# Kernel tuning notes

Hardware: AMD Instinct MI355X
Metric: run time of the kernel (lower is better)

Reference implementation:

```python
import jax, jax.numpy as jnp
import numpy as np


def setup_inputs() -> dict:
    key = jax.random.key(0)
    ks = jax.random.split(key, 7)
    B, C, W, H = 4, 256, 64, 64
    C8 = C // 8
    return {
        "x": jax.random.normal(ks[0], (B, C, W, H), dtype=jnp.float32),
        "Wq": jax.random.normal(ks[1], (C8, C), dtype=jnp.float32) * 0.05,
        "bq": jax.random.normal(ks[2], (C8,), dtype=jnp.float32) * 0.05,
        "Wk": jax.random.normal(ks[3], (C8, C), dtype=jnp.float32) * 0.05,
        "bk": jax.random.normal(ks[4], (C8,), dtype=jnp.float32) * 0.05,
        "Wv": jax.random.normal(ks[5], (C, C), dtype=jnp.float32) * 0.05,
        "bv": jax.random.normal(ks[6], (C,), dtype=jnp.float32) * 0.05,
    }


def reference(x, Wq, bq, Wk, bk, Wv, bv):
    B, C, W, H = x.shape
    N = W * H
    xf = x.reshape(B, C, N)  # flatten spatial dims
    # 1x1 convs == per-position linear projections
    q = jnp.einsum('oc,bcn->bno', Wq, xf) + bq            # (B, N, C/8)
    k = jnp.einsum('oc,bcn->bon', Wk, xf) + bk[None, :, None]  # (B, C/8, N)
    # attention scores (B, N, N); original applies softmax over dim=1
    attn = jax.nn.softmax(jnp.einsum('bno,bom->bnm', q, k), axis=1)
    v = jnp.einsum('oc,bcn->bno', Wv, xf) + bv            # (B, N, C)
    out = jnp.einsum('bnm,bmc->bnc', attn, v)             # (B, N, C)
    # faithful to original: raw view of (B, N, C) as (B, C, W, H)
    return out.reshape(B, C, W, H)
```

## Files before the change

kernel.cpp:

```cpp
#include <hip/hip_runtime.h>
#include <math.h>

#define NB 4
#define CC 256
#define CO 32
#define NN 4096
#define MU 320
#define LOG2E 1.44269504088896f

typedef __attribute__((ext_vector_type(4))) float f4;
typedef __attribute__((ext_vector_type(8))) short s8;
typedef __attribute__((ext_vector_type(8))) unsigned short us8;
typedef __attribute__((ext_vector_type(2))) unsigned int u2;
typedef __attribute__((ext_vector_type(4))) unsigned int u4i;

__device__ __forceinline__ unsigned short f2bf(float f) {
    unsigned int u = __float_as_uint(f);
    u = (u + 0x7FFFu + ((u >> 16) & 1u)) >> 16;
    return (unsigned short)u;
}
__device__ __forceinline__ unsigned int cvtpk(float lo, float hi) {
    unsigned int r;
    asm("v_cvt_pk_bf16_f32 %0, %1, %2" : "=v"(r) : "v"(lo), "v"(hi));
    return r;
}
__device__ __forceinline__ int swz128(int row, int colByte) {
    return row * 128 + (colByte ^ ((row & 7) << 4));
}

union s8u4 { s8 s; u4i u; };

__global__ __launch_bounds__(256) void prepw_kernel(
    const float* __restrict__ Wq, const float* __restrict__ bq,
    const float* __restrict__ Wk, const float* __restrict__ bk,
    const float* __restrict__ Wv, const float* __restrict__ bv,
    unsigned short* __restrict__ Wb, float* __restrict__ fb)
{
    const int t = threadIdx.x;
    #pragma unroll
    for (int i = 0; i < 4; ++i) {
        const int e = blockIdx.x * 1024 + i * 256 + t;
        const int u = e >> 8, c = e & 255;
        float val = (u < 32) ? Wq[u * 256 + c]
                  : (u < 64) ? Wk[(u - 32) * 256 + c]
                             : Wv[(u - 64) * 256 + c];
        Wb[e] = f2bf(val);
    }
    if (blockIdx.x == 0) {
        for (int u = t; u < MU; u += 256)
            fb[u] = (u < 32) ? bq[u] : (u < 64) ? bk[u - 32] : bv[u - 64];
    }
}

__global__ __launch_bounds__(256) void projf_kernel(
    const float* __restrict__ x, const unsigned short* __restrict__ Wb,
    const float* __restrict__ fb,
    unsigned short* __restrict__ qb, unsigned short* __restrict__ kb,
    unsigned short* __restrict__ vtb)
{
    __shared__ float xl[32][260];

    const int t   = threadIdx.x;
    const int b   = blockIdx.x >> 7;
    const int nbl = blockIdx.x & 127;
    const int n0  = nbl * 32;

    {
        const int nl = t & 7;
        const int c8 = t >> 3;
        #pragma unroll
        for (int pass = 0; pass < 8; ++pass) {
            const int c = c8 + pass * 32;
            f4 xv = *reinterpret_cast<const f4*>(x + ((size_t)(b * CC + c)) * NN + n0 + nl * 4);
            #pragma unroll
            for (int j = 0; j < 4; ++j) xl[nl * 4 + j][c] = xv[j];
        }
    }
    __syncthreads();

    const int w    = t >> 6;
    const int l    = t & 63;
    const int l15  = l & 15;
    const int g4   = l >> 4;
    const int nw   = w & 1;
    const int uw   = w >> 1;
    const int nloc = nw * 16 + l15;
    const int n    = n0 + nloc;

    s8 bfr[8];
    #pragma unroll
    for (int kk = 0; kk < 8; ++kk) {
        f4 a  = *reinterpret_cast<const f4*>(&xl[nloc][kk * 32 + g4 * 8]);
        f4 c2 = *reinterpret_cast<const f4*>(&xl[nloc][kk * 32 + g4 * 8 + 4]);
        s8u4 tmp;
        tmp.u = (u4i){ cvtpk(a[0], a[1]), cvtpk(a[2], a[3]),
                       cvtpk(c2[0], c2[1]), cvtpk(c2[2], c2[3]) };
        bfr[kk] = tmp.s;
    }

    const f4 z = {0.f, 0.f, 0.f, 0.f};
    unsigned short* qrow = qb + ((size_t)(b * NN + n)) * CO;
    unsigned short* krow = kb + ((size_t)(b * NN + n)) * CO;

    #pragma unroll
    for (int i = 0; i < 10; ++i) {
        const int u0 = (uw * 10 + i) * 16;
        f4 acc = z;
        #pragma unroll
        for (int kk = 0; kk < 8; ++kk) {
            s8 af = *reinterpret_cast<const s8*>(Wb + (size_t)(u0 + l15) * CC + kk * 32 + g4 * 8);
            acc = __builtin_amdgcn_mfma_f32_16x16x32_bf16(af, bfr[kk], acc, 0, 0, 0);
        }
        f4 bias4 = *reinterpret_cast<const f4*>(fb + u0 + g4 * 4);
        if (u0 < 32) {
            u2 pw = { cvtpk((acc[0] + bias4[0]) * LOG2E, (acc[1] + bias4[1]) * LOG2E),
                      cvtpk((acc[2] + bias4[2]) * LOG2E, (acc[3] + bias4[3]) * LOG2E) };
            *reinterpret_cast<u2*>(qrow + u0 + g4 * 4) = pw;
        } else if (u0 < 64) {
            u2 pw = { cvtpk(acc[0] + bias4[0], acc[1] + bias4[1]),
                      cvtpk(acc[2] + bias4[2], acc[3] + bias4[3]) };
            *reinterpret_cast<u2*>(krow + (u0 - 32) + g4 * 4) = pw;
        } else {
            const int cbase = u0 - 64 + g4 * 4;
            #pragma unroll
            for (int r = 0; r < 4; ++r)
                vtb[((size_t)(b * CC + cbase + r)) * NN + n] = f2bf(acc[r] + bias4[r]);
        }
    }
}

__global__ __launch_bounds__(256) void colstats_kernel(
    const unsigned short* __restrict__ qb, const unsigned short* __restrict__ kb,
    unsigned short* __restrict__ vtb)
{
    __shared__ float red[4][16];
    __shared__ float civl[16];

    const int t   = threadIdx.x;
    const int b   = blockIdx.x >> 8;
    const int mb  = blockIdx.x & 255;
    const int l   = t & 63;
    const int w   = t >> 6;
    const int l15 = l & 15;
    const int g4  = l >> 4;
    const int m   = mb * 16 + l15;

    const unsigned short* qbB = qb + (size_t)b * NN * CO;
    s8 kfrag = *reinterpret_cast<const s8*>(kb + ((size_t)b * NN + m) * CO + g4 * 8);

    const f4 z = {0.f, 0.f, 0.f, 0.f};
    float ssum = 0.f;

    const int nbeg = w * 1024, nend = nbeg + 1024;
    for (int n0 = nbeg; n0 < nend; n0 += 32) {
        s8 a0 = *reinterpret_cast<const s8*>(qbB + (size_t)(n0 + l15) * CO + g4 * 8);
        s8 a1 = *reinterpret_cast<const s8*>(qbB + (size_t)(n0 + 16 + l15) * CO + g4 * 8);
        f4 d0 = __builtin_amdgcn_mfma_f32_16x16x32_bf16(a0, kfrag, z, 0, 0, 0);
        f4 d1 = __builtin_amdgcn_mfma_f32_16x16x32_bf16(a1, kfrag, z, 0, 0, 0);
        #pragma unroll
        for (int r = 0; r < 4; ++r) ssum += exp2f(d0[r]) + exp2f(d1[r]);
    }

    ssum += __shfl_xor(ssum, 16);
    ssum += __shfl_xor(ssum, 32);
    if (l < 16) red[w][l15] = ssum;
    __syncthreads();
    if (w == 0 && l < 16)
        civl[l15] = 1.0f / (red[0][l15] + red[1][l15] + red[2][l15] + red[3][l15]);
    __syncthreads();

    unsigned short* vp = vtb + ((size_t)(b * CC + t)) * NN + mb * 16;
    #pragma unroll
    for (int i = 0; i < 2; ++i) {
        us8 vv = *reinterpret_cast<const us8*>(vp + i * 8);
        u4i o;
        #pragma unroll
        for (int e2 = 0; e2 < 4; ++e2) {
            float f0 = __uint_as_float((unsigned int)vv[2 * e2]     << 16) * civl[i * 8 + 2 * e2];
            float f1 = __uint_as_float((unsigned int)vv[2 * e2 + 1] << 16) * civl[i * 8 + 2 * e2 + 1];
            o[e2] = cvtpk(f0, f1);
        }
        *reinterpret_cast<u4i*>(vp + i * 8) = o;
    }
}

__global__ __launch_bounds__(512) void attn_kernel(
    const unsigned short* __restrict__ qb, const unsigned short* __restrict__ kb,
    const unsigned short* __restrict__ vtb, float* __restrict__ out)
{
    __shared__ __align__(16) char plds[2][64 * 128];
    __shared__ __align__(16) char vlds[2][128 * 128];

    const int t    = threadIdx.x;
    const int bid  = blockIdx.x;
    const int cblk = bid & 1;
    const int nblk = (bid >> 1) & 63;
    const int b    = bid >> 7;
    const int n0   = nblk * 64;
    const int c0   = cblk * 128;
    const int l    = t & 63;
    const int w    = t >> 6;
    const int l15  = l & 15;
    const int g4   = l >> 4;
    const int g    = w >> 1;
    const int p    = w & 1;
    const int wrn  = w >> 2;
    const int wcq  = w & 3;

    const unsigned short* qbB = qb  + (size_t)b * NN * CO;
    const unsigned short* kbB = kb  + (size_t)b * NN * CO;
    const unsigned short* vtB = vtb + (size_t)b * CC * NN;

    s8 qfrag = *reinterpret_cast<const s8*>(qbB + (size_t)(n0 + g * 16 + l15) * CO + g4 * 8);

    const int vrow = t >> 2;
    const int q4   = t & 3;
    const int pw0  = swz128(g * 16 + l15, (2 * p) * 32 + g4 * 8);
    const int pw1  = swz128(g * 16 + l15, (2 * p + 1) * 32 + g4 * 8);
    const int vw0  = swz128(vrow, q4 * 32);
    const int vw1  = swz128(vrow, q4 * 32 + 16);
    const int prk0a0 = swz128(wrn * 32 +      l15,      g4 * 16);
    const int prk0a1 = swz128(wrn * 32 + 16 + l15,      g4 * 16);
    const int prk1a0 = swz128(wrn * 32 +      l15, 64 + g4 * 16);
    const int prk1a1 = swz128(wrn * 32 + 16 + l15, 64 + g4 * 16);
    const int vrk0c0 = swz128(wcq * 32 +      l15,      g4 * 16);
    const int vrk0c1 = swz128(wcq * 32 + 16 + l15,      g4 * 16);
    const int vrk1c0 = swz128(wcq * 32 +      l15, 64 + g4 * 16);
    const int vrk1c1 = swz128(wcq * 32 + 16 + l15, 64 + g4 * 16);

    const unsigned short* kp = kbB + (size_t)((2 * p) * 16 + l15) * CO + g4 * 8;
    const unsigned short* vp = vtB + (size_t)(c0 + vrow) * NN + q4 * 16;

    s8 kreg[2];
    s8 vs[2];
    const f4 z = {0.f, 0.f, 0.f, 0.f};

#define LOADNEXT() do { \
        kreg[0] = *reinterpret_cast<const s8*>(kp); \
        kreg[1] = *reinterpret_cast<const s8*>(kp + 16 * CO); \
        vs[0]   = *reinterpret_cast<const s8*>(vp); \
        vs[1]   = *reinterpret_cast<const s8*>(vp + 8); \
        kp += 64 * CO; vp += 64; \
    } while (0)

#define STAGE(BUF) do { \
        f4 d0 = __builtin_amdgcn_mfma_f32_16x16x32_bf16(kreg[0], qfrag, z, 0, 0, 0); \
        f4 d1 = __builtin_amdgcn_mfma_f32_16x16x32_bf16(kreg[1], qfrag, z, 0, 0, 0); \
        u2 pq0 = { cvtpk(exp2f(d0[0]), exp2f(d0[1])), cvtpk(exp2f(d0[2]), exp2f(d0[3])) }; \
        u2 pq1 = { cvtpk(exp2f(d1[0]), exp2f(d1[1])), cvtpk(exp2f(d1[2]), exp2f(d1[3])) }; \
        *reinterpret_cast<u2*>(plds[BUF] + pw0) = pq0; \
        *reinterpret_cast<u2*>(plds[BUF] + pw1) = pq1; \
        *reinterpret_cast<s8*>(vlds[BUF] + vw0) = vs[0]; \
        *reinterpret_cast<s8*>(vlds[BUF] + vw1) = vs[1]; \
    } while (0)

#define PVSTEP(BUF) do { \
        s8 pa00 = *reinterpret_cast<const s8*>(plds[BUF] + prk0a0); \
        s8 pa01 = *reinterpret_cast<const s8*>(plds[BUF] + prk0a1); \
        s8 pa10 = *reinterpret_cast<const s8*>(plds[BUF] + prk1a0); \
        s8 pa11 = *reinterpret_cast<const s8*>(plds[BUF] + prk1a1); \
        s8 vb00 = *reinterpret_cast<const s8*>(vlds[BUF] + vrk0c0); \
        s8 vb01 = *reinterpret_cast<const s8*>(vlds[BUF] + vrk0c1); \
        s8 vb10 = *reinterpret_cast<const s8*>(vlds[BUF] + vrk1c0); \
        s8 vb11 = *reinterpret_cast<const s8*>(vlds[BUF] + vrk1c1); \
        __builtin_amdgcn_s_setprio(1); \
        acc[0][0] = __builtin_amdgcn_mfma_f32_16x16x32_bf16(pa00, vb00, acc[0][0], 0, 0, 0); \
        acc[0][1] = __builtin_amdgcn_mfma_f32_16x16x32_bf16(pa00, vb01, acc[0][1], 0, 0, 0); \
        acc[1][0] = __builtin_amdgcn_mfma_f32_16x16x32_bf16(pa01, vb00, acc[1][0], 0, 0, 0); \
        acc[1][1] = __builtin_amdgcn_mfma_f32_16x16x32_bf16(pa01, vb01, acc[1][1], 0, 0, 0); \
        acc[0][0] = __builtin_amdgcn_mfma_f32_16x16x32_bf16(pa10, vb10, acc[0][0], 0, 0, 0); \
        acc[0][1] = __builtin_amdgcn_mfma_f32_16x16x32_bf16(pa10, vb11, acc[0][1], 0, 0, 0); \
        acc[1][0] = __builtin_amdgcn_mfma_f32_16x16x32_bf16(pa11, vb10, acc[1][0], 0, 0, 0); \
        acc[1][1] = __builtin_amdgcn_mfma_f32_16x16x32_bf16(pa11, vb11, acc[1][1], 0, 0, 0); \
        __builtin_amdgcn_s_setprio(0); \
    } while (0)

    f4 acc[2][2];
    acc[0][0] = z; acc[0][1] = z; acc[1][0] = z; acc[1][1] = z;

    LOADNEXT();
    STAGE(0);
    LOADNEXT();
    __syncthreads();

    for (int i = 0; i < 64; i += 2) {
        if (i < 63) {
            STAGE(1);
            if (i < 62) LOADNEXT();
        }
        PVSTEP(0);
        __syncthreads();
        if (i + 1 < 63) {
            STAGE(0);
            if (i + 1 < 62) LOADNEXT();
        }
        PVSTEP(1);
        __syncthreads();
    }

#undef LOADNEXT
#undef STAGE
#undef PVSTEP

    #pragma unroll
    for (int a = 0; a < 2; ++a) {
        const int row = n0 + wrn * 32 + a * 16 + g4 * 4;
        #pragma unroll
        for (int c = 0; c < 2; ++c) {
            const int col = c0 + wcq * 32 + c * 16 + l15;
            #pragma unroll
            for (int r = 0; r < 4; ++r)
                out[((size_t)(b * NN + row + r)) * CC + col] = acc[a][c][r];
        }
    }
}

extern "C" void kernel_launch(void* const* d_in, const int* in_sizes, int n_in,
                              void* d_out, int out_size, void* d_ws, size_t ws_size,
                              hipStream_t stream)
{
    const float* x  = (const float*)d_in[0];
    const float* Wq = (const float*)d_in[1];
    const float* bq = (const float*)d_in[2];
    const float* Wk = (const float*)d_in[3];
    const float* bk = (const float*)d_in[4];
    const float* Wv = (const float*)d_in[5];
    const float* bv = (const float*)d_in[6];
    float* out = (float*)d_out;

    unsigned short* qb  = (unsigned short*)d_ws;
    unsigned short* kb  = qb + (size_t)NB * NN * CO;
    unsigned short* vtb = kb + (size_t)NB * NN * CO;
    unsigned short* Wb  = vtb + (size_t)NB * CC * NN;
    float*          fb  = (float*)(Wb + (size_t)MU * CC);

    prepw_kernel<<<dim3(80), dim3(256), 0, stream>>>(Wq, bq, Wk, bk, Wv, bv, Wb, fb);
    projf_kernel<<<dim3(512), dim3(256), 0, stream>>>(x, Wb, fb, qb, kb, vtb);
    colstats_kernel<<<dim3(1024), dim3(256), 0, stream>>>(qb, kb, vtb);
    attn_kernel<<<dim3(512), dim3(512), 0, stream>>>(qb, kb, vtb, out);
}
```

Before: 127.2 us.

## Pre-swizzle V into MFMA fragment layout and load directly to registers

The column-normalization kernel now writes the scaled V into a separate buffer laid out in the exact per-lane MFMA B-operand fragment order. The attention kernel then loads V fragments straight from global memory into registers, double-buffered across iterations, and drops the V shared-memory staging and its LDS reads and writes. This removes LDS traffic and bank pressure for V at the cost of more global/L2 loads per wave (each wave reloads its own fragments), an extra workspace buffer, and more registers.

```diff
diff --git a/kernel.cpp b/kernel.cpp
--- a/kernel.cpp
+++ b/kernel.cpp
@@ -131,7 +131,7 @@
 
 __global__ __launch_bounds__(256) void colstats_kernel(
     const unsigned short* __restrict__ qb, const unsigned short* __restrict__ kb,
-    unsigned short* __restrict__ vtb)
+    const unsigned short* __restrict__ vtb, unsigned short* __restrict__ vfr)
 {
     __shared__ float red[4][16];
     __shared__ float civl[16];
@@ -169,7 +169,15 @@
         civl[l15] = 1.0f / (red[0][l15] + red[1][l15] + red[2][l15] + red[3][l15]);
     __syncthreads();
 
-    unsigned short* vp = vtb + ((size_t)(b * CC + t)) * NN + mb * 16;
+    const int mt   = mb >> 2;
+    const int ksl  = (mb >> 1) & 1;
+    const int g4b  = (mb & 1) * 2;
+    const int cg   = t >> 4;
+    const int l15v = t & 15;
+    const unsigned short* vp = vtb + ((size_t)(b * CC + t)) * NN + mb * 16;
+    unsigned short* dst = vfr + (size_t)b * 1048576
+                        + (((mt * 16 + cg) * 2 + ksl) << 9)
+                        + (g4b * 16 + l15v) * 8;
     #pragma unroll
     for (int i = 0; i < 2; ++i) {
         us8 vv = *reinterpret_cast<const us8*>(vp + i * 8);
@@ -180,16 +188,15 @@
             float f1 = __uint_as_float((unsigned int)vv[2 * e2 + 1] << 16) * civl[i * 8 + 2 * e2 + 1];
             o[e2] = cvtpk(f0, f1);
         }
-        *reinterpret_cast<u4i*>(vp + i * 8) = o;
+        *reinterpret_cast<u4i*>(dst + i * 128) = o;
     }
 }
 
 __global__ __launch_bounds__(512) void attn_kernel(
     const unsigned short* __restrict__ qb, const unsigned short* __restrict__ kb,
-    const unsigned short* __restrict__ vtb, float* __restrict__ out)
+    const unsigned short* __restrict__ vfr, float* __restrict__ out)
 {
     __shared__ __align__(16) char plds[2][64 * 128];
-    __shared__ __align__(16) char vlds[2][128 * 128];
 
     const int t    = threadIdx.x;
     const int bid  = blockIdx.x;
@@ -209,38 +216,36 @@
 
     const unsigned short* qbB = qb  + (size_t)b * NN * CO;
     const unsigned short* kbB = kb  + (size_t)b * NN * CO;
-    const unsigned short* vtB = vtb + (size_t)b * CC * NN;
 
     s8 qfrag = *reinterpret_cast<const s8*>(qbB + (size_t)(n0 + g * 16 + l15) * CO + g4 * 8);
 
-    const int vrow = t >> 2;
-    const int q4   = t & 3;
     const int pw0  = swz128(g * 16 + l15, (2 * p) * 32 + g4 * 8);
     const int pw1  = swz128(g * 16 + l15, (2 * p + 1) * 32 + g4 * 8);
-    const int vw0  = swz128(vrow, q4 * 32);
-    const int vw1  = swz128(vrow, q4 * 32 + 16);
     const int prk0a0 = swz128(wrn * 32 +      l15,      g4 * 16);
     const int prk0a1 = swz128(wrn * 32 + 16 + l15,      g4 * 16);
     const int prk1a0 = swz128(wrn * 32 +      l15, 64 + g4 * 16);
     const int prk1a1 = swz128(wrn * 32 + 16 + l15, 64 + g4 * 16);
-    const int vrk0c0 = swz128(wcq * 32 +      l15,      g4 * 16);
-    const int vrk0c1 = swz128(wcq * 32 + 16 + l15,      g4 * 16);
-    const int vrk1c0 = swz128(wcq * 32 +      l15, 64 + g4 * 16);
-    const int vrk1c1 = swz128(wcq * 32 + 16 + l15, 64 + g4 * 16);
-
-    const unsigned short* kp = kbB + (size_t)((2 * p) * 16 + l15) * CO + g4 * 8;
-    const unsigned short* vp = vtB + (size_t)(c0 + vrow) * NN + q4 * 16;
+
+    const unsigned short* kp  = kbB + (size_t)((2 * p) * 16 + l15) * CO + g4 * 8;
+    const unsigned short* vpf = vfr + (size_t)b * 1048576
+                              + (size_t)((c0 >> 4) + wcq * 2) * 1024 + l * 8;
 
     s8 kreg[2];
-    s8 vs[2];
+    s8 vA0, vA1, vA2, vA3, vB0, vB1, vB2, vB3;
     const f4 z = {0.f, 0.f, 0.f, 0.f};
 
-#define LOADNEXT() do { \
+#define LOADK() do { \
         kreg[0] = *reinterpret_cast<const s8*>(kp); \
         kreg[1] = *reinterpret_cast<const s8*>(kp + 16 * CO); \
-        vs[0]   = *reinterpret_cast<const s8*>(vp); \
-        vs[1]   = *reinterpret_cast<const s8*>(vp + 8); \
-        kp += 64 * CO; vp += 64; \
+        kp += 64 * CO; \
+    } while (0)
+
+#define LOADVB(V0, V1, V2, V3) do { \
+        V0 = *reinterpret_cast<const s8*>(vpf); \
+        V1 = *reinterpret_cast<const s8*>(vpf + 512); \
+        V2 = *reinterpret_cast<const s8*>(vpf + 1024); \
+        V3 = *reinterpret_cast<const s8*>(vpf + 1536); \
+        vpf += 16384; \
     } while (0)
 
 #define STAGE(BUF) do { \
@@ -250,55 +255,55 @@
         u2 pq1 = { cvtpk(exp2f(d1[0]), exp2f(d1[1])), cvtpk(exp2f(d1[2]), exp2f(d1[3])) }; \
         *reinterpret_cast<u2*>(plds[BUF] + pw0) = pq0; \
         *reinterpret_cast<u2*>(plds[BUF] + pw1) = pq1; \
-        *reinterpret_cast<s8*>(vlds[BUF] + vw0) = vs[0]; \
-        *reinterpret_cast<s8*>(vlds[BUF] + vw1) = vs[1]; \
     } while (0)
 
-#define PVSTEP(BUF) do { \
+#define PVSTEP(BUF, V0, V1, V2, V3) do { \
         s8 pa00 = *reinterpret_cast<const s8*>(plds[BUF] + prk0a0); \
         s8 pa01 = *reinterpret_cast<const s8*>(plds[BUF] + prk0a1); \
         s8 pa10 = *reinterpret_cast<const s8*>(plds[BUF] + prk1a0); \
         s8 pa11 = *reinterpret_cast<const s8*>(plds[BUF] + prk1a1); \
-        s8 vb00 = *reinterpret_cast<const s8*>(vlds[BUF] + vrk0c0); \
-        s8 vb01 = *reinterpret_cast<const s8*>(vlds[BUF] + vrk0c1); \
-        s8 vb10 = *reinterpret_cast<const s8*>(vlds[BUF] + vrk1c0); \
-        s8 vb11 = *reinterpret_cast<const s8*>(vlds[BUF] + vrk1c1); \
         __builtin_amdgcn_s_setprio(1); \
-        acc[0][0] = __builtin_amdgcn_mfma_f32_16x16x32_bf16(pa00, vb00, acc[0][0], 0, 0, 0); \
-        acc[0][1] = __builtin_amdgcn_mfma_f32_16x16x32_bf16(pa00, vb01, acc[0][1], 0, 0, 0); \
-        acc[1][0] = __builtin_amdgcn_mfma_f32_16x16x32_bf16(pa01, vb00, acc[1][0], 0, 0, 0); \
-        acc[1][1] = __builtin_amdgcn_mfma_f32_16x16x32_bf16(pa01, vb01, acc[1][1], 0, 0, 0); \
-        acc[0][0] = __builtin_amdgcn_mfma_f32_16x16x32_bf16(pa10, vb10, acc[0][0], 0, 0, 0); \
-        acc[0][1] = __builtin_amdgcn_mfma_f32_16x16x32_bf16(pa10, vb11, acc[0][1], 0, 0, 0); \
-        acc[1][0] = __builtin_amdgcn_mfma_f32_16x16x32_bf16(pa11, vb10, acc[1][0], 0, 0, 0); \
-        acc[1][1] = __builtin_amdgcn_mfma_f32_16x16x32_bf16(pa11, vb11, acc[1][1], 0, 0, 0); \
+        acc[0][0] = __builtin_amdgcn_mfma_f32_16x16x32_bf16(pa00, V0, acc[0][0], 0, 0, 0); \
+        acc[0][1] = __builtin_amdgcn_mfma_f32_16x16x32_bf16(pa00, V2, acc[0][1], 0, 0, 0); \
+        acc[1][0] = __builtin_amdgcn_mfma_f32_16x16x32_bf16(pa01, V0, acc[1][0], 0, 0, 0); \
+        acc[1][1] = __builtin_amdgcn_mfma_f32_16x16x32_bf16(pa01, V2, acc[1][1], 0, 0, 0); \
+        acc[0][0] = __builtin_amdgcn_mfma_f32_16x16x32_bf16(pa10, V1, acc[0][0], 0, 0, 0); \
+        acc[0][1] = __builtin_amdgcn_mfma_f32_16x16x32_bf16(pa10, V3, acc[0][1], 0, 0, 0); \
+        acc[1][0] = __builtin_amdgcn_mfma_f32_16x16x32_bf16(pa11, V1, acc[1][0], 0, 0, 0); \
+        acc[1][1] = __builtin_amdgcn_mfma_f32_16x16x32_bf16(pa11, V3, acc[1][1], 0, 0, 0); \
         __builtin_amdgcn_s_setprio(0); \
     } while (0)
 
     f4 acc[2][2];
     acc[0][0] = z; acc[0][1] = z; acc[1][0] = z; acc[1][1] = z;
 
-    LOADNEXT();
+    LOADK();
+    LOADVB(vA0, vA1, vA2, vA3);
     STAGE(0);
-    LOADNEXT();
+    LOADK();
+    LOADVB(vB0, vB1, vB2, vB3);
     __syncthreads();
 
     for (int i = 0; i < 64; i += 2) {
         if (i < 63) {
             STAGE(1);
-            if (i < 62) LOADNEXT();
-        }
-        PVSTEP(0);
+            if (i < 62) LOADK();
+        }
+        PVSTEP(0, vA0, vA1, vA2, vA3);
+        if (i < 62) LOADVB(vA0, vA1, vA2, vA3);
         __syncthreads();
+
         if (i + 1 < 63) {
             STAGE(0);
-            if (i + 1 < 62) LOADNEXT();
-        }
-        PVSTEP(1);
+            if (i + 1 < 62) LOADK();
+        }
+        PVSTEP(1, vB0, vB1, vB2, vB3);
+        if (i + 1 < 62) LOADVB(vB0, vB1, vB2, vB3);
         __syncthreads();
     }
 
-#undef LOADNEXT
+#undef LOADK
+#undef LOADVB
 #undef STAGE
 #undef PVSTEP
 
@@ -329,13 +334,14 @@
     float* out = (float*)d_out;
 
     unsigned short* qb  = (unsigned short*)d_ws;
-    unsigned short* kb  = qb + (size_t)NB * NN * CO;
-    unsigned short* vtb = kb + (size_t)NB * NN * CO;
-    unsigned short* Wb  = vtb + (size_t)NB * CC * NN;
+    unsigned short* kb  = qb  + (size_t)NB * NN * CO;
+    unsigned short* vtb = kb  + (size_t)NB * NN * CO;
+    unsigned short* vfr = vtb + (size_t)NB * CC * NN;
+    unsigned short* Wb  = vfr + (size_t)NB * CC * NN;
     float*          fb  = (float*)(Wb + (size_t)MU * CC);
 
     prepw_kernel<<<dim3(80), dim3(256), 0, stream>>>(Wq, bq, Wk, bk, Wv, bv, Wb, fb);
     projf_kernel<<<dim3(512), dim3(256), 0, stream>>>(x, Wb, fb, qb, kb, vtb);
-    colstats_kernel<<<dim3(1024), dim3(256), 0, stream>>>(qb, kb, vtb);
-    attn_kernel<<<dim3(512), dim3(512), 0, stream>>>(qb, kb, vtb, out);
-}
+    colstats_kernel<<<dim3(1024), dim3(256), 0, stream>>>(qb, kb, vtb, vfr);
+    attn_kernel<<<dim3(512), dim3(512), 0, stream>>>(qb, kb, vfr, out);
+}
```

Measured after the change: 122.3 us. 3.8% less time.
